# Kernel optimization log

Hardware: AMD Instinct MI355X
Metric: run time of the kernel (lower is better)

## Reference

```python
import jax, jax.numpy as jnp
import numpy as np

EPS = 1e-6
LN_EPS = 1e-5

def _ln(x, g, b):
    m = x.mean(-1, keepdims=True)
    v = x.var(-1, keepdims=True)
    return (x - m) / jnp.sqrt(v + LN_EPS) * g + b

def _gelu(x):
    return jax.nn.gelu(x, approximate=False)  # torch nn.GELU default (erf)

def _compress(x, W1, b1, g1, B1, W2, b2, g2, B2, W3, b3):
    h = _ln(_gelu(x @ W1 + b1), g1, B1)
    h = _ln(_gelu(h @ W2 + b2), g2, B2)
    return h @ W3 + b3

def _decompress(x, W1, b1, g1, B1, W2, b2, g2, B2, W3, b3):
    h = _ln(_gelu(x @ W1 + b1), g1, B1)
    h = _ln(_gelu(h @ W2 + b2), g2, B2)
    return h @ W3 + b3

def setup_inputs() -> dict:
    key = jax.random.key(0)
    ks = jax.random.split(key, 12)
    B, D, C, N = 1024, 1024, 256, 100000
    s = 0.02
    return {
        "query": jax.random.normal(ks[0], (B, D), jnp.float32),
        "keys_c": jax.random.normal(ks[1], (N, C), jnp.float32),
        "values_c": jax.random.normal(ks[2], (N, C), jnp.float32),
        "cW1": jax.random.normal(ks[3], (D, D // 2), jnp.float32) * s,
        "cb1": jnp.zeros((D // 2,), jnp.float32),
        "cg1": jnp.ones((D // 2,), jnp.float32),
        "cB1": jnp.zeros((D // 2,), jnp.float32),
        "cW2": jax.random.normal(ks[4], (D // 2, D // 4), jnp.float32) * s,
        "cb2": jnp.zeros((D // 4,), jnp.float32),
        "cg2": jnp.ones((D // 4,), jnp.float32),
        "cB2": jnp.zeros((D // 4,), jnp.float32),
        "cW3": jax.random.normal(ks[5], (D // 4, C), jnp.float32) * s,
        "cb3": jnp.zeros((C,), jnp.float32),
        "dW1": jax.random.normal(ks[6], (C, D // 4), jnp.float32) * s,
        "db1": jnp.zeros((D // 4,), jnp.float32),
        "dg1": jnp.ones((D // 4,), jnp.float32),
        "dB1": jnp.zeros((D // 4,), jnp.float32),
        "dW2": jax.random.normal(ks[7], (D // 4, D // 2), jnp.float32) * s,
        "db2": jnp.zeros((D // 2,), jnp.float32),
        "dg2": jnp.ones((D // 2,), jnp.float32),
        "dB2": jnp.zeros((D // 2,), jnp.float32),
        "dW3": jax.random.normal(ks[8], (D // 2, D), jnp.float32) * s,
        "db3": jnp.zeros((D,), jnp.float32),
        "k": 5,
    }

def reference(query, keys_c, values_c,
              cW1, cb1, cg1, cB1, cW2, cb2, cg2, cB2, cW3, cb3,
              dW1, db1, dg1, dB1, dW2, db2, dg2, dB2, dW3, db3, k):
    # compress query: [B, D] -> [B, C]
    q_c = _compress(query, cW1, cb1, cg1, cB1, cW2, cb2, cg2, cB2, cW3, cb3)
    # brute-force squared-L2 distances (FAISS IndexFlatL2 semantics): [B, N]
    q2 = jnp.sum(q_c * q_c, axis=-1, keepdims=True)
    k2 = jnp.sum(keys_c * keys_c, axis=-1)[None, :]
    d = jnp.maximum(q2 + k2 - 2.0 * (q_c @ keys_c.T), 0.0)
    # top-k nearest (smallest distances), sorted ascending
    neg_d, idx = jax.lax.top_k(-d, k)  # [B, k]
    d_top = -neg_d
    # inverse-distance weights, normalized per query
    w = 1.0 / (d_top + EPS)
    w = w / jnp.sum(w, axis=-1, keepdims=True)
    # gather stored compressed values and decompress: [B, k, C] -> [B, k, D]
    v = values_c[idx]
    dec = _decompress(v, dW1, db1, dg1, dB1, dW2, db2, dg2, dB2, dW3, db3)
    retrieved = jnp.einsum('bk,bkd->bd', w, dec)
    confidence = 1.0 / (d_top[:, 0] + EPS)  # min distance is first (sorted)
    return retrieved, confidence
```

## Files before the change

### kernel.cpp

```cpp
#include <hip/hip_runtime.h>
#include <cfloat>
#include <cstddef>

typedef __attribute__((ext_vector_type(8))) short bf16x8;
typedef __attribute__((ext_vector_type(4))) float f32x4;

#define NKEYS    100000
#define SPLITS   61
#define SPLITLEN 1664
#define NKP      (SPLITS * SPLITLEN)
#define NCHUNK   (SPLITLEN / 128)
#define PREPB    (NKP / 4)
#define CSPLB    1024
#define WSPB     352

__device__ __forceinline__ unsigned short f2bf(float x) {
    unsigned int u = __float_as_uint(x);
    unsigned int r = (u + 0x7fffu + ((u >> 16) & 1u)) >> 16;
    return (unsigned short)r;
}
__device__ __forceinline__ float bf2f(unsigned short h) {
    return __uint_as_float((unsigned)h << 16);
}
__device__ __forceinline__ void split2(float x, unsigned short& h, unsigned short& l) {
    h = f2bf(x);
    float r = x - bf2f(h);
    l = f2bf(r);
}

__device__ __forceinline__ void async16(void* lds, const void* g) {
    __builtin_amdgcn_global_load_lds(
        (const __attribute__((address_space(1))) unsigned int*)g,
        (__attribute__((address_space(3))) unsigned int*)lds, 16, 0, 0);
}

__device__ __forceinline__ unsigned pack_si(float sc, unsigned local) {
    unsigned u = __float_as_uint(sc);
    unsigned m = u ^ ((unsigned)((int)u >> 31) | 0x80000000u);
    return (m & 0xFFFFF800u) | local;
}

__device__ __forceinline__ void chain5(unsigned (&a)[5], unsigned v) {
    #pragma unroll
    for (int i = 0; i < 5; ++i) {
        unsigned t = min(a[i], v);
        a[i] = max(a[i], v);
        v = t;
    }
}
__device__ __forceinline__ void ins5u(unsigned (&a)[5], unsigned v) {
    if (__any((int)(v > a[4]))) chain5(a, v);
}

__device__ __forceinline__ void ins8p(unsigned (&s)[8], int (&ix)[8], unsigned v, int vi) {
    if (v > s[7]) {
        s[7] = v; ix[7] = vi;
        #pragma unroll
        for (int i = 7; i > 0; --i) {
            if (s[i] > s[i - 1]) {
                unsigned tv = s[i]; s[i] = s[i - 1]; s[i - 1] = tv;
                int ti = ix[i]; ix[i] = ix[i - 1]; ix[i - 1] = ti;
            }
        }
    }
}

__global__ __launch_bounds__(256, 2) void mfma_gemm(
    const unsigned short* __restrict__ Ahi, const unsigned short* __restrict__ Alo,
    const unsigned short* __restrict__ Whi, const unsigned short* __restrict__ Wlo,
    const float* __restrict__ bias, float* __restrict__ C,
    int M, int N, int K, int do_gelu)
{
    __shared__ unsigned short sT[2][8192];
    const int tid = threadIdx.x;
    const int lane = tid & 63;
    const int wv = tid >> 6;
    const int wr = wv >> 1, wc = wv & 1;
    const int m0 = blockIdx.y << 6, n0 = blockIdx.x << 6;

    const int rl = lane & 15, kq = (lane >> 4) << 3;
    const unsigned short* sp[4];
    sp[0] = Ahi + (size_t)(m0 + (wv << 4) + rl) * K + kq;
    sp[1] = Alo + (size_t)(m0 + (wv << 4) + rl) * K + kq;
    sp[2] = Whi + (size_t)(n0 + (wv << 4) + rl) * K + kq;
    sp[3] = Wlo + (size_t)(n0 + (wv << 4) + rl) * K + kq;
    const int ldss = (wv << 9) | (lane << 3);

    f32x4 acc[2][2];
    #pragma unroll
    for (int p = 0; p < 2; ++p)
        #pragma unroll
        for (int q = 0; q < 2; ++q) acc[p][q] = (f32x4){0.f, 0.f, 0.f, 0.f};

    const int steps = K >> 5;
    #pragma unroll
    for (int i = 0; i < 4; ++i)
        async16(&sT[0][(i << 11) + ldss], sp[i]);

    for (int s = 0; s < steps; ++s) {
        const int cur = s & 1;
        __syncthreads();
        if (s + 1 < steps) {
            const int ko = (s + 1) << 5;
            #pragma unroll
            for (int i = 0; i < 4; ++i)
                async16(&sT[cur ^ 1][(i << 11) + ldss], sp[i] + ko);
        }
        bf16x8 ah[2], al[2], wh[2], wl[2];
        #pragma unroll
        for (int p = 0; p < 2; ++p) {
            ah[p] = *(const bf16x8*)&sT[cur][(((wr << 1) + p) << 9) | (lane << 3)];
            al[p] = *(const bf16x8*)&sT[cur][2048 + ((((wr << 1) + p) << 9) | (lane << 3))];
        }
        #pragma unroll
        for (int q = 0; q < 2; ++q) {
            wh[q] = *(const bf16x8*)&sT[cur][4096 + ((((wc << 1) + q) << 9) | (lane << 3))];
            wl[q] = *(const bf16x8*)&sT[cur][6144 + ((((wc << 1) + q) << 9) | (lane << 3))];
        }
        #pragma unroll
        for (int p = 0; p < 2; ++p)
            #pragma unroll
            for (int q = 0; q < 2; ++q) {
                acc[p][q] = __builtin_amdgcn_mfma_f32_16x16x32_bf16(ah[p], wh[q], acc[p][q], 0, 0, 0);
                acc[p][q] = __builtin_amdgcn_mfma_f32_16x16x32_bf16(ah[p], wl[q], acc[p][q], 0, 0, 0);
                acc[p][q] = __builtin_amdgcn_mfma_f32_16x16x32_bf16(al[p], wh[q], acc[p][q], 0, 0, 0);
            }
    }

    #pragma unroll
    for (int q = 0; q < 2; ++q) {
        const int n = n0 + (((wc << 1) + q) << 4) + (lane & 15);
        const float bn = bias[n];
        #pragma unroll
        for (int p = 0; p < 2; ++p) {
            #pragma unroll
            for (int j = 0; j < 4; ++j) {
                const int m = m0 + (((wr << 1) + p) << 4) + ((lane >> 4) << 2) + j;
                float v = acc[p][q][j] + bn;
                if (do_gelu) v = 0.5f * v * (1.0f + erff(v * 0.70710678118654752f));
                C[(size_t)m * N + n] = v;
            }
        }
    }
}

__device__ __forceinline__ void wsplit_tile(
    const float* __restrict__ W, unsigned short* __restrict__ Thi,
    unsigned short* __restrict__ Tlo, int K, int N, int n0, int k0, int tid)
{
    __shared__ float tile[64][65];
    const int nl = tid & 63, kg = tid >> 6;
    #pragma unroll
    for (int r = 0; r < 16; ++r)
        tile[kg + (r << 2)][nl] = W[(size_t)(k0 + kg + (r << 2)) * N + n0 + nl];
    __syncthreads();
    const int nn = tid >> 2, kc = (tid & 3) << 4;
    unsigned short* ph = Thi + (size_t)(n0 + nn) * K + k0 + kc;
    unsigned short* pl = Tlo + (size_t)(n0 + nn) * K + k0 + kc;
    #pragma unroll
    for (int c = 0; c < 16; c += 4) {
        ushort4 H, L;
        split2(tile[kc + c + 0][nn], H.x, L.x);
        split2(tile[kc + c + 1][nn], H.y, L.y);
        split2(tile[kc + c + 2][nn], H.z, L.z);
        split2(tile[kc + c + 3][nn], H.w, L.w);
        *(ushort4*)(ph + c) = H;
        *(ushort4*)(pl + c) = L;
    }
}

__device__ __forceinline__ void prep_group(
    const float* __restrict__ X, unsigned short* __restrict__ xh,
    float* __restrict__ x2, int nvalid, int grp, int tid)
{
    const int row = (grp << 2) + (tid >> 6);
    const int lane = tid & 63;
    if (row < nvalid) {
        float4 v = *(const float4*)(X + ((size_t)row << 8) + (lane << 2));
        float ss = v.x * v.x + v.y * v.y + v.z * v.z + v.w * v.w;
        #pragma unroll
        for (int off = 32; off > 0; off >>= 1) ss += __shfl_xor(ss, off);
        ushort4 h;
        h.x = f2bf(v.x); h.y = f2bf(v.y); h.z = f2bf(v.z); h.w = f2bf(v.w);
        *(ushort4*)(xh + ((size_t)row << 8) + (lane << 2)) = h;
        if (lane == 0) x2[row] = ss;
    } else {
        ushort4 z = {0, 0, 0, 0};
        *(ushort4*)(xh + ((size_t)row << 8) + (lane << 2)) = z;
        if (lane == 0) x2[row] = FLT_MAX;
    }
}

__global__ __launch_bounds__(256) void prep_all(
    const float* __restrict__ keys, unsigned short* __restrict__ khi, float* __restrict__ k2,
    const float* __restrict__ query, unsigned short* __restrict__ qsh, unsigned short* __restrict__ qsl,
    const float* __restrict__ cW1, const float* __restrict__ cW2, const float* __restrict__ cW3,
    const float* __restrict__ dW1, const float* __restrict__ dW2, const float* __restrict__ dW3,
    unsigned short* wc1h, unsigned short* wc1l, unsigned short* wc2h, unsigned short* wc2l,
    unsigned short* wc3h, unsigned short* wc3l, unsigned short* wd1h, unsigned short* wd1l,
    unsigned short* wd2h, unsigned short* wd2l, unsigned short* wd3h, unsigned short* wd3l)
{
    const int bid = blockIdx.x;
    const int tid = threadIdx.x;
    if (bid < PREPB) {
        prep_group(keys, khi, k2, NKEYS, bid, tid);
        return;
    }
    if (bid < PREPB + CSPLB) {
        const size_t i = ((size_t)(bid - PREPB) * 256 + tid) << 2;
        float4 v = *(const float4*)(query + i);
        ushort4 H, L;
        split2(v.x, H.x, L.x);
        split2(v.y, H.y, L.y);
        split2(v.z, H.z, L.z);
        split2(v.w, H.w, L.w);
        *(ushort4*)(qsh + i) = H;
        *(ushort4*)(qsl + i) = L;
        return;
    }
    int t = bid - (PREPB + CSPLB);
    const float* W; unsigned short *Th, *Tl; int K, N;
    if (t < 128)      {          W = cW1; Th = wc1h; Tl = wc1l; K = 1024; N = 512;  }
    else if (t < 160) { t -= 128; W = cW2; Th = wc2h; Tl = wc2l; K = 512;  N = 256;  }
    else if (t < 176) { t -= 160; W = cW3; Th = wc3h; Tl = wc3l; K = 256;  N = 256;  }
    else if (t < 192) { t -= 176; W = dW1; Th = wd1h; Tl = wd1l; K = 256;  N = 256;  }
    else if (t < 224) { t -= 192; W = dW2; Th = wd2h; Tl = wd2l; K = 256;  N = 512;  }
    else              { t -= 224; W = dW3; Th = wd3h; Tl = wd3l; K = 512;  N = 1024; }
    const int nx = N >> 6;
    wsplit_tile(W, Th, Tl, K, N, (t % nx) << 6, (t / nx) << 6, tid);
}

__global__ __launch_bounds__(256) void prep_q(
    const float* __restrict__ X, unsigned short* __restrict__ xh, float* __restrict__ x2)
{
    prep_group(X, xh, x2, 1024, blockIdx.x, threadIdx.x);
}

__global__ __launch_bounds__(256) void ln_rows(
    float* __restrict__ X, const float* __restrict__ g, const float* __restrict__ b, int C)
{
    const int row = blockIdx.x;
    const int tid = threadIdx.x;
    float* xr = X + (size_t)row * C;
    float v0 = xr[tid];
    float v1 = (C > 256) ? xr[tid + 256] : 0.0f;
    float s = v0 + v1;
    float ss = v0 * v0 + v1 * v1;
    #pragma unroll
    for (int off = 32; off > 0; off >>= 1) {
        s  += __shfl_xor(s, off);
        ss += __shfl_xor(ss, off);
    }
    __shared__ float red[10];
    const int wave = tid >> 6, lane = tid & 63;
    if (lane == 0) { red[wave] = s; red[wave + 4] = ss; }
    __syncthreads();
    if (tid == 0) {
        float S  = red[0] + red[1] + red[2] + red[3];
        float SS = red[4] + red[5] + red[6] + red[7];
        float m = S / C;
        float var = SS / C - m * m;
        red[8] = m;
        red[9] = 1.0f / sqrtf(var + 1e-5f);
    }
    __syncthreads();
    float m = red[8], inv = red[9];
    xr[tid] = (v0 - m) * inv * g[tid] + b[tid];
    if (C > 256) xr[tid + 256] = (v1 - m) * inv * g[tid + 256] + b[tid + 256];
}

__global__ __launch_bounds__(256) void ln_split(
    const float* __restrict__ X, const float* __restrict__ g, const float* __restrict__ b,
    int C, unsigned short* __restrict__ hi, unsigned short* __restrict__ lo)
{
    const int row = blockIdx.x;
    const int tid = threadIdx.x;
    const float* xr = X + (size_t)row * C;
    float v0 = xr[tid];
    float v1 = (C > 256) ? xr[tid + 256] : 0.0f;
    float s = v0 + v1;
    float ss = v0 * v0 + v1 * v1;
    #pragma unroll
    for (int off = 32; off > 0; off >>= 1) {
        s  += __shfl_xor(s, off);
        ss += __shfl_xor(ss, off);
    }
    __shared__ float red[10];
    const int wave = tid >> 6, lane = tid & 63;
    if (lane == 0) { red[wave] = s; red[wave + 4] = ss; }
    __syncthreads();
    if (tid == 0) {
        float S  = red[0] + red[1] + red[2] + red[3];
        float SS = red[4] + red[5] + red[6] + red[7];
        float m = S / C;
        float var = SS / C - m * m;
        red[8] = m;
        red[9] = 1.0f / sqrtf(var + 1e-5f);
    }
    __syncthreads();
    float m = red[8], inv = red[9];
    {
        float y = (v0 - m) * inv * g[tid] + b[tid];
        unsigned short h, l; split2(y, h, l);
        hi[(size_t)row * C + tid] = h;
        lo[(size_t)row * C + tid] = l;
    }
    if (C > 256) {
        float y = (v1 - m) * inv * g[tid + 256] + b[tid + 256];
        unsigned short h, l; split2(y, h, l);
        hi[(size_t)row * C + tid + 256] = h;
        lo[(size_t)row * C + tid + 256] = l;
    }
}

__global__ __launch_bounds__(256, 2) void dist_topk_mfma(
    const unsigned short* __restrict__ khi, const unsigned short* __restrict__ qhi,
    const float* __restrict__ k2, unsigned* __restrict__ cand_p)
{
    __shared__ unsigned short sB[2][8192];
    const int tid = threadIdx.x;
    const int lane = tid & 63;
    const int wv = tid >> 6;

    const int fid = blockIdx.x;
    const int rr = fid & 7, row = fid >> 3;
    int split, jq;
    if (row < 56) { split = rr * 7 + (row >> 3); jq = row & 7; }
    else { int slot = ((row - 56) << 3) + rr; split = 56 + (slot >> 3); jq = slot & 7; }
    const int kstart = split * SPLITLEN;
    const int q0 = jq * 128 + wv * 32;

    bf16x8 aF[2][8];
    #pragma unroll
    for (int qt = 0; qt < 2; ++qt) {
        const unsigned short* qb = qhi
            + (((size_t)(q0 + qt * 16 + (lane & 15))) << 8) + ((lane >> 4) << 3);
        #pragma unroll
        for (int s = 0; s < 8; ++s) aF[qt][s] = *(const bf16x8*)(qb + s * 32);
    }

    size_t soff[4];
    int ldst[4];
    #pragma unroll
    for (int i = 0; i < 4; ++i) {
        int e = i * 256 + tid;
        int h = e >> 9, t = (e >> 6) & 7, L = e & 63;
        soff[i] = (((size_t)(kstart + t * 16 + (L & 15))) << 8)
                + (h << 5) + ((L >> 4) << 3);
        ldst[i] = e << 3;
    }

    unsigned bp[2][4][5];
    #pragma unroll
    for (int qt = 0; qt < 2; ++qt)
        #pragma unroll
        for (int r = 0; r < 4; ++r)
            #pragma unroll
            for (int j = 0; j < 5; ++j) bp[qt][r][j] = 0u;

    #pragma unroll
    for (int i = 0; i < 4; ++i)
        async16(&sB[0][ldst[i]], khi + soff[i]);

    int cur = 0;
    for (int c = 0; c < NCHUNK; ++c) {
        const int coff = c << 15;
        f32x4 acc[2][8];
        #pragma unroll
        for (int qt = 0; qt < 2; ++qt)
            #pragma unroll
            for (int t = 0; t < 8; ++t) acc[qt][t] = (f32x4){0.f, 0.f, 0.f, 0.f};

        #pragma unroll
        for (int st = 0; st < 4; ++st) {
            __syncthreads();
            const int g = (c << 2) + st;
            if (g + 1 < NCHUNK * 4) {
                const int ns = (st + 1) & 3;
                const int ncoff = (st == 3) ? (coff + 32768) : coff;
                #pragma unroll
                for (int i = 0; i < 4; ++i)
                    async16(&sB[cur ^ 1][ldst[i]],
                            khi + soff[i] + (size_t)(ncoff + (ns << 6)));
            }
            #pragma unroll
            for (int h = 0; h < 2; ++h) {
                #pragma unroll
                for (int t = 0; t < 8; ++t) {
                    bf16x8 b = *(const bf16x8*)
                        &sB[cur][((((h << 3) + t) << 6) | lane) << 3];
                    acc[0][t] = __builtin_amdgcn_mfma_f32_16x16x32_bf16(
                        aF[0][(st << 1) + h], b, acc[0][t], 0, 0, 0);
                    acc[1][t] = __builtin_amdgcn_mfma_f32_16x16x32_bf16(
                        aF[1][(st << 1) + h], b, acc[1][t], 0, 0, 0);
                }
            }
            cur ^= 1;
        }

        const int kb = c << 7;
        #pragma unroll
        for (int t = 0; t < 8; ++t) {
            const unsigned local = (unsigned)(kb + t * 16 + (lane & 15));
            const float k2v = k2[kstart + (int)local];
            #pragma unroll
            for (int qt = 0; qt < 2; ++qt)
                #pragma unroll
                for (int r = 0; r < 4; ++r) {
                    float sc = fmaf(-0.5f, k2v, acc[qt][t][r]);
                    ins5u(bp[qt][r], pack_si(sc, local));
                }
        }
    }

    #pragma unroll
    for (int m = 1; m <= 8; m <<= 1) {
        #pragma unroll
        for (int qt = 0; qt < 2; ++qt)
            #pragma unroll
            for (int r = 0; r < 4; ++r) {
                unsigned o[5];
                #pragma unroll
                for (int j = 0; j < 5; ++j)
                    o[j] = (unsigned)__shfl_xor((int)bp[qt][r][j], m);
                #pragma unroll
                for (int j = 0; j < 5; ++j) ins5u(bp[qt][r], o[j]);
            }
    }
    if ((lane & 15) == 0) {
        #pragma unroll
        for (int qt = 0; qt < 2; ++qt)
            #pragma unroll
            for (int r = 0; r < 4; ++r) {
                const int q = q0 + qt * 16 + ((lane >> 4) << 2) + r;
                #pragma unroll
                for (int j = 0; j < 5; ++j)
                    cand_p[(size_t)(split * 5 + j) * 1024 + q] = bp[qt][r][j];
            }
    }
}

__global__ __launch_bounds__(256) void mrg_rank_gather(
    const unsigned* __restrict__ cand_p,
    const float* __restrict__ qc, const float* __restrict__ keys,
    const float* __restrict__ k2, const float* __restrict__ q2,
    float* __restrict__ w5, float* __restrict__ conf,
    const float* __restrict__ values,
    unsigned short* __restrict__ x0h, unsigned short* __restrict__ x0l)
{
    const int tid = threadIdx.x;
    const int lane = tid & 63;
    const int q = (blockIdx.x << 2) + (tid >> 6);

    unsigned fp[8]; int fi[8];
    #pragma unroll
    for (int j = 0; j < 8; ++j) { fp[j] = 0u; fi[j] = 0; }
    for (int t = lane; t < SPLITS * 5; t += 64) {
        unsigned v = cand_p[(size_t)t * 1024 + q];
        ins8p(fp, fi, v, (t / 5) * SPLITLEN + (int)(v & 2047u));
    }
    #pragma unroll
    for (int m = 1; m <= 32; m <<= 1) {
        unsigned op[8]; int oi[8];
        #pragma unroll
        for (int j = 0; j < 8; ++j) {
            op[j] = (unsigned)__shfl_xor((int)fp[j], m);
            oi[j] = __shfl_xor(fi[j], m);
        }
        #pragma unroll
        for (int j = 0; j < 8; ++j) ins8p(fp, fi, op[j], oi[j]);
    }

    const float4 qv = *(const float4*)(qc + ((size_t)q << 8) + (lane << 2));
    float dot[8];
    #pragma unroll
    for (int c = 0; c < 8; ++c) {
        const float4 kv = *(const float4*)(keys + ((size_t)fi[c] << 8) + (lane << 2));
        dot[c] = qv.x * kv.x + qv.y * kv.y + qv.z * kv.z + qv.w * kv.w;
    }
    #pragma unroll
    for (int c = 0; c < 8; ++c)
        #pragma unroll
        for (int off = 32; off > 0; off >>= 1) dot[c] += __shfl_xor(dot[c], off);
    float d[8]; int di[8];
    const float qq = q2[q];
    #pragma unroll
    for (int c = 0; c < 8; ++c) {
        d[c] = fmaxf(qq + k2[fi[c]] - 2.0f * dot[c], 0.0f);
        di[c] = fi[c];
    }
    #pragma unroll
    for (int a = 1; a < 8; ++a) {
        float dv = d[a]; int iv = di[a]; int b = a;
        while (b > 0 && d[b - 1] > dv) { d[b] = d[b - 1]; di[b] = di[b - 1]; --b; }
        d[b] = dv; di[b] = iv;
    }
    float w[5], sum = 0.0f;
    #pragma unroll
    for (int j = 0; j < 5; ++j) { w[j] = 1.0f / (d[j] + 1e-6f); sum += w[j]; }
    if (lane == 0) {
        #pragma unroll
        for (int j = 0; j < 5; ++j) w5[q * 5 + j] = w[j] / sum;
        conf[q] = 1.0f / (d[0] + 1e-6f);
    }

    #pragma unroll
    for (int j = 0; j < 5; ++j) {
        const size_t r = (size_t)q * 5 + j;
        const float4 v = *(const float4*)(values + ((size_t)di[j] << 8) + (lane << 2));
        ushort4 H, L;
        split2(v.x, H.x, L.x);
        split2(v.y, H.y, L.y);
        split2(v.z, H.z, L.z);
        split2(v.w, H.w, L.w);
        *(ushort4*)(x0h + (r << 8) + (lane << 2)) = H;
        *(ushort4*)(x0l + (r << 8) + (lane << 2)) = L;
    }
}

__global__ __launch_bounds__(128) void combine_split(
    const float* __restrict__ h2d, const float* __restrict__ w5,
    unsigned short* __restrict__ zhi, unsigned short* __restrict__ zlo)
{
    const int q = blockIdx.x;
    const int t = threadIdx.x;
    float4 acc = {0.0f, 0.0f, 0.0f, 0.0f};
    #pragma unroll
    for (int i = 0; i < 5; ++i) {
        float w = w5[q * 5 + i];
        float4 v = *(const float4*)(h2d + ((size_t)q * 5 + i) * 512 + (t << 2));
        acc.x = fmaf(w, v.x, acc.x);
        acc.y = fmaf(w, v.y, acc.y);
        acc.z = fmaf(w, v.z, acc.z);
        acc.w = fmaf(w, v.w, acc.w);
    }
    ushort4 H, L;
    split2(acc.x, H.x, L.x);
    split2(acc.y, H.y, L.y);
    split2(acc.z, H.z, L.z);
    split2(acc.w, H.w, L.w);
    *(ushort4*)(zhi + (size_t)q * 512 + (t << 2)) = H;
    *(ushort4*)(zlo + (size_t)q * 512 + (t << 2)) = L;
}

#define OFF_KHI 0
#define OFF_K2  12992512
#define OFF_QHI 13094016
#define OFF_Q2  13225088
#define OFF_QC  13226112
#define OFF_CP  13488256
#define OFF_W5  13808768
#define OFF_WT  13819008
#define OFF_UN  15260800

#define W_C1H 0
#define W_C1L 262144
#define W_C2H 524288
#define W_C2L 589824
#define W_C3H 655360
#define W_C3L 688128
#define W_D1H 720896
#define W_D1L 753664
#define W_D2H 786432
#define W_D2L 851968
#define W_D3H 917504
#define W_D3L 1179648

#define U_H1   0
#define U_H1H  524288
#define U_H1L  786432
#define U_H2   1048576
#define U_H2H  1310720
#define U_H2L  1441792
#define U_QSH  1572864
#define U_QSL  2097152
#define U_X0H  0
#define U_X0L  655360
#define U_T1   1310720
#define U_T1H  2621440
#define U_T1L  3276800
#define U_T2   3932160
#define U_ZH   6553600
#define U_ZL   6815744

extern "C" void kernel_launch(void* const* d_in, const int* in_sizes, int n_in,
                              void* d_out, int out_size, void* d_ws, size_t ws_size,
                              hipStream_t stream) {
    const float* query  = (const float*)d_in[0];
    const float* keys   = (const float*)d_in[1];
    const float* values = (const float*)d_in[2];
    const float* cW1 = (const float*)d_in[3];  const float* cb1 = (const float*)d_in[4];
    const float* cg1 = (const float*)d_in[5];  const float* cB1 = (const float*)d_in[6];
    const float* cW2 = (const float*)d_in[7];  const float* cb2 = (const float*)d_in[8];
    const float* cg2 = (const float*)d_in[9];  const float* cB2 = (const float*)d_in[10];
    const float* cW3 = (const float*)d_in[11]; const float* cb3 = (const float*)d_in[12];
    const float* dW1 = (const float*)d_in[13]; const float* db1 = (const float*)d_in[14];
    const float* dg1 = (const float*)d_in[15]; const float* dB1 = (const float*)d_in[16];
    const float* dW2 = (const float*)d_in[17]; const float* db2 = (const float*)d_in[18];
    const float* dg2 = (const float*)d_in[19]; const float* dB2 = (const float*)d_in[20];
    const float* dW3 = (const float*)d_in[21]; const float* db3 = (const float*)d_in[22];
    float* out = (float*)d_out;
    float* ws  = (float*)d_ws;

    unsigned short* khi = (unsigned short*)(ws + OFF_KHI);
    float* k2 = ws + OFF_K2;
    unsigned short* qhi = (unsigned short*)(ws + OFF_QHI);
    float* q2 = ws + OFF_Q2;
    float* qc = ws + OFF_QC;
    unsigned* cand_p = (unsigned*)(ws + OFF_CP);
    float* w5 = ws + OFF_W5;
    float* wt = ws + OFF_WT;
    float* un = ws + OFF_UN;

    unsigned short* wc1h = (unsigned short*)(wt + W_C1H);
    unsigned short* wc1l = (unsigned short*)(wt + W_C1L);
    unsigned short* wc2h = (unsigned short*)(wt + W_C2H);
    unsigned short* wc2l = (unsigned short*)(wt + W_C2L);
    unsigned short* wc3h = (unsigned short*)(wt + W_C3H);
    unsigned short* wc3l = (unsigned short*)(wt + W_C3L);
    unsigned short* wd1h = (unsigned short*)(wt + W_D1H);
    unsigned short* wd1l = (unsigned short*)(wt + W_D1L);
    unsigned short* wd2h = (unsigned short*)(wt + W_D2H);
    unsigned short* wd2l = (unsigned short*)(wt + W_D2L);
    unsigned short* wd3h = (unsigned short*)(wt + W_D3H);
    unsigned short* wd3l = (unsigned short*)(wt + W_D3L);

    float* h1 = un + U_H1;
    unsigned short* h1h = (unsigned short*)(un + U_H1H);
    unsigned short* h1l = (unsigned short*)(un + U_H1L);
    float* h2 = un + U_H2;
    unsigned short* h2h = (unsigned short*)(un + U_H2H);
    unsigned short* h2l = (unsigned short*)(un + U_H2L);
    unsigned short* qsh = (unsigned short*)(un + U_QSH);
    unsigned short* qsl = (unsigned short*)(un + U_QSL);
    unsigned short* x0h = (unsigned short*)(un + U_X0H);
    unsigned short* x0l = (unsigned short*)(un + U_X0L);
    float* t1 = un + U_T1;
    unsigned short* t1h = (unsigned short*)(un + U_T1H);
    unsigned short* t1l = (unsigned short*)(un + U_T1L);
    float* t2 = un + U_T2;
    unsigned short* zh = (unsigned short*)(un + U_ZH);
    unsigned short* zl = (unsigned short*)(un + U_ZL);
    float* conf = out + 1024 * 1024;

    prep_all<<<PREPB + CSPLB + WSPB, 256, 0, stream>>>(
        keys, khi, k2, query, qsh, qsl,
        cW1, cW2, cW3, dW1, dW2, dW3,
        wc1h, wc1l, wc2h, wc2l, wc3h, wc3l, wd1h, wd1l, wd2h, wd2l, wd3h, wd3l);

    mfma_gemm<<<dim3(8, 16),  256, 0, stream>>>(qsh, qsl, wc1h, wc1l, cb1, h1, 1024, 512, 1024, 1);
    ln_split<<<1024, 256, 0, stream>>>(h1, cg1, cB1, 512, h1h, h1l);
    mfma_gemm<<<dim3(4, 16),  256, 0, stream>>>(h1h, h1l, wc2h, wc2l, cb2, h2, 1024, 256, 512, 1);
    ln_split<<<1024, 256, 0, stream>>>(h2, cg2, cB2, 256, h2h, h2l);
    mfma_gemm<<<dim3(4, 16),  256, 0, stream>>>(h2h, h2l, wc3h, wc3l, cb3, qc, 1024, 256, 256, 0);
    prep_q<<<256, 256, 0, stream>>>(qc, qhi, q2);

    dist_topk_mfma<<<SPLITS * 8, 256, 0, stream>>>(khi, qhi, k2, cand_p);
    mrg_rank_gather<<<256, 256, 0, stream>>>(cand_p, qc, keys, k2, q2, w5, conf,
                                             values, x0h, x0l);

    mfma_gemm<<<dim3(4, 80),  256, 0, stream>>>(x0h, x0l, wd1h, wd1l, db1, t1, 5120, 256, 256, 1);
    ln_split<<<5120, 256, 0, stream>>>(t1, dg1, dB1, 256, t1h, t1l);
    mfma_gemm<<<dim3(8, 80),  256, 0, stream>>>(t1h, t1l, wd2h, wd2l, db2, t2, 5120, 512, 256, 1);
    ln_rows<<<5120, 256, 0, stream>>>(t2, dg2, dB2, 512);
    combine_split<<<1024, 128, 0, stream>>>(t2, w5, zh, zl);
    mfma_gemm<<<dim3(16, 16), 256, 0, stream>>>(zh, zl, wd3h, wd3l, db3, out, 1024, 1024, 512, 0);
}
```

Before: 495.5 us.

## Split key scan into more shorter chunks and fuse decoder LayerNorm with weighted combine

The brute-force distance/top-k scan now uses 112 splits of 896 keys instead of 61 splits of 1664. This raises block count and parallelism across CUs, with a simpler block-to-split mapping, at the cost of more candidates to merge per query. Separately, the second decoder LayerNorm and the weighted combine over the k neighbours are fused into one kernel, removing a full write and reread of the 5120x512 intermediate. Buffer offsets are recomputed for the larger candidate array.

New measurement: 509.7 us. +2.8%, slower.

```diff
diff --git a/kernel.cpp b/kernel.cpp
--- a/kernel.cpp
+++ b/kernel.cpp
@@ -6,10 +6,11 @@
 typedef __attribute__((ext_vector_type(4))) float f32x4;
 
 #define NKEYS    100000
-#define SPLITS   61
-#define SPLITLEN 1664
+#define SPLITS   112
+#define SPLITLEN 896
 #define NKP      (SPLITS * SPLITLEN)
 #define NCHUNK   (SPLITLEN / 128)
+#define NCAND    (SPLITS * 5)
 #define PREPB    (NKP / 4)
 #define CSPLB    1024
 #define WSPB     352
@@ -236,12 +237,13 @@
     prep_group(X, xh, x2, 1024, blockIdx.x, threadIdx.x);
 }
 
-__global__ __launch_bounds__(256) void ln_rows(
-    float* __restrict__ X, const float* __restrict__ g, const float* __restrict__ b, int C)
+__global__ __launch_bounds__(256) void ln_split(
+    const float* __restrict__ X, const float* __restrict__ g, const float* __restrict__ b,
+    int C, unsigned short* __restrict__ hi, unsigned short* __restrict__ lo)
 {
     const int row = blockIdx.x;
     const int tid = threadIdx.x;
-    float* xr = X + (size_t)row * C;
+    const float* xr = X + (size_t)row * C;
     float v0 = xr[tid];
     float v1 = (C > 256) ? xr[tid + 256] : 0.0f;
     float s = v0 + v1;
@@ -265,40 +267,6 @@
     }
     __syncthreads();
     float m = red[8], inv = red[9];
-    xr[tid] = (v0 - m) * inv * g[tid] + b[tid];
-    if (C > 256) xr[tid + 256] = (v1 - m) * inv * g[tid + 256] + b[tid + 256];
-}
-
-__global__ __launch_bounds__(256) void ln_split(
-    const float* __restrict__ X, const float* __restrict__ g, const float* __restrict__ b,
-    int C, unsigned short* __restrict__ hi, unsigned short* __restrict__ lo)
-{
-    const int row = blockIdx.x;
-    const int tid = threadIdx.x;
-    const float* xr = X + (size_t)row * C;
-    float v0 = xr[tid];
-    float v1 = (C > 256) ? xr[tid + 256] : 0.0f;
-    float s = v0 + v1;
-    float ss = v0 * v0 + v1 * v1;
-    #pragma unroll
-    for (int off = 32; off > 0; off >>= 1) {
-        s  += __shfl_xor(s, off);
-        ss += __shfl_xor(ss, off);
-    }
-    __shared__ float red[10];
-    const int wave = tid >> 6, lane = tid & 63;
-    if (lane == 0) { red[wave] = s; red[wave + 4] = ss; }
-    __syncthreads();
-    if (tid == 0) {
-        float S  = red[0] + red[1] + red[2] + red[3];
-        float SS = red[4] + red[5] + red[6] + red[7];
-        float m = S / C;
-        float var = SS / C - m * m;
-        red[8] = m;
-        red[9] = 1.0f / sqrtf(var + 1e-5f);
-    }
-    __syncthreads();
-    float m = red[8], inv = red[9];
     {
         float y = (v0 - m) * inv * g[tid] + b[tid];
         unsigned short h, l; split2(y, h, l);
@@ -313,6 +281,50 @@
     }
 }
 
+__global__ __launch_bounds__(256) void ln_combine(
+    const float* __restrict__ X, const float* __restrict__ g, const float* __restrict__ b,
+    const float* __restrict__ w5, unsigned short* __restrict__ zhi,
+    unsigned short* __restrict__ zlo)
+{
+    const int q = blockIdx.x, tid = threadIdx.x;
+    const int wave = tid >> 6, lane = tid & 63;
+    __shared__ float red[10];
+    float a0 = 0.f, a1 = 0.f;
+    for (int i = 0; i < 5; ++i) {
+        const float* xr = X + ((size_t)q * 5 + i) * 512;
+        float v0 = xr[tid], v1 = xr[tid + 256];
+        float s = v0 + v1, ss = v0 * v0 + v1 * v1;
+        #pragma unroll
+        for (int off = 32; off > 0; off >>= 1) {
+            s  += __shfl_xor(s, off);
+            ss += __shfl_xor(ss, off);
+        }
+        if (lane == 0) { red[wave] = s; red[wave + 4] = ss; }
+        __syncthreads();
+        if (tid == 0) {
+            float S  = red[0] + red[1] + red[2] + red[3];
+            float SS = red[4] + red[5] + red[6] + red[7];
+            float m = S / 512.0f;
+            float var = SS / 512.0f - m * m;
+            red[8] = m;
+            red[9] = 1.0f / sqrtf(var + 1e-5f);
+        }
+        __syncthreads();
+        const float m = red[8], inv = red[9];
+        const float w = w5[q * 5 + i];
+        a0 = fmaf(w, (v0 - m) * inv * g[tid] + b[tid], a0);
+        a1 = fmaf(w, (v1 - m) * inv * g[tid + 256] + b[tid + 256], a1);
+        __syncthreads();
+    }
+    unsigned short h, l;
+    split2(a0, h, l);
+    zhi[(size_t)q * 512 + tid] = h;
+    zlo[(size_t)q * 512 + tid] = l;
+    split2(a1, h, l);
+    zhi[(size_t)q * 512 + tid + 256] = h;
+    zlo[(size_t)q * 512 + tid + 256] = l;
+}
+
 __global__ __launch_bounds__(256, 2) void dist_topk_mfma(
     const unsigned short* __restrict__ khi, const unsigned short* __restrict__ qhi,
     const float* __restrict__ k2, unsigned* __restrict__ cand_p)
@@ -323,10 +335,9 @@
     const int wv = tid >> 6;
 
     const int fid = blockIdx.x;
-    const int rr = fid & 7, row = fid >> 3;
-    int split, jq;
-    if (row < 56) { split = rr * 7 + (row >> 3); jq = row & 7; }
-    else { int slot = ((row - 56) << 3) + rr; split = 56 + (slot >> 3); jq = slot & 7; }
+    const int x = fid & 7, y = fid >> 3;
+    const int split = ((y >> 3) << 3) + x;
+    const int jq = y & 7;
     const int kstart = split * SPLITLEN;
     const int q0 = jq * 128 + wv * 32;
 
@@ -455,7 +466,7 @@
     unsigned fp[8]; int fi[8];
     #pragma unroll
     for (int j = 0; j < 8; ++j) { fp[j] = 0u; fi[j] = 0; }
-    for (int t = lane; t < SPLITS * 5; t += 64) {
+    for (int t = lane; t < NCAND; t += 64) {
         unsigned v = cand_p[(size_t)t * 1024 + q];
         ins8p(fp, fi, v, (t / 5) * SPLITLEN + (int)(v & 2047u));
     }
@@ -518,40 +529,15 @@
     }
 }
 
-__global__ __launch_bounds__(128) void combine_split(
-    const float* __restrict__ h2d, const float* __restrict__ w5,
-    unsigned short* __restrict__ zhi, unsigned short* __restrict__ zlo)
-{
-    const int q = blockIdx.x;
-    const int t = threadIdx.x;
-    float4 acc = {0.0f, 0.0f, 0.0f, 0.0f};
-    #pragma unroll
-    for (int i = 0; i < 5; ++i) {
-        float w = w5[q * 5 + i];
-        float4 v = *(const float4*)(h2d + ((size_t)q * 5 + i) * 512 + (t << 2));
-        acc.x = fmaf(w, v.x, acc.x);
-        acc.y = fmaf(w, v.y, acc.y);
-        acc.z = fmaf(w, v.z, acc.z);
-        acc.w = fmaf(w, v.w, acc.w);
-    }
-    ushort4 H, L;
-    split2(acc.x, H.x, L.x);
-    split2(acc.y, H.y, L.y);
-    split2(acc.z, H.z, L.z);
-    split2(acc.w, H.w, L.w);
-    *(ushort4*)(zhi + (size_t)q * 512 + (t << 2)) = H;
-    *(ushort4*)(zlo + (size_t)q * 512 + (t << 2)) = L;
-}
-
 #define OFF_KHI 0
-#define OFF_K2  12992512
-#define OFF_QHI 13094016
-#define OFF_Q2  13225088
-#define OFF_QC  13226112
-#define OFF_CP  13488256
-#define OFF_W5  13808768
-#define OFF_WT  13819008
-#define OFF_UN  15260800
+#define OFF_K2  12845056
+#define OFF_QHI 12945408
+#define OFF_Q2  13076480
+#define OFF_QC  13077504
+#define OFF_CP  13339648
+#define OFF_W5  13913088
+#define OFF_WT  13918208
+#define OFF_UN  15360000
 
 #define W_C1H 0
 #define W_C1L 262144
@@ -662,7 +648,6 @@
     mfma_gemm<<<dim3(4, 80),  256, 0, stream>>>(x0h, x0l, wd1h, wd1l, db1, t1, 5120, 256, 256, 1);
     ln_split<<<5120, 256, 0, stream>>>(t1, dg1, dB1, 256, t1h, t1l);
     mfma_gemm<<<dim3(8, 80),  256, 0, stream>>>(t1h, t1l, wd2h, wd2l, db2, t2, 5120, 512, 256, 1);
-    ln_rows<<<5120, 256, 0, stream>>>(t2, dg2, dB2, 512);
-    combine_split<<<1024, 128, 0, stream>>>(t2, w5, zh, zl);
+    ln_combine<<<1024, 256, 0, stream>>>(t2, dg2, dB2, w5, zh, zl);
     mfma_gemm<<<dim3(16, 16), 256, 0, stream>>>(zh, zl, wd3h, wd3l, db3, out, 1024, 1024, 512, 0);
 }
```
